# Kernel optimization log

Measured on AMD Instinct MI355X. Metric: run time of the kernel, lower is better.

## Reference

```python
import jax, jax.numpy as jnp
import numpy as np

N_SEARCH, B, C, H, W = 10, 32, 768, 24, 24
HT, WT = 8, 8
HEADS, POOL = 12, 4


def _G(t):
    # Integral of the bilinear triangle kernel: G(t) = int_{-1}^{t} max(0,1-|s|) ds
    tc = jnp.clip(t, -1.0, 1.0)
    return 0.5 + tc * (1.0 - 0.5 * jnp.abs(tc))


def prroi_pool(feats, rois, pool):
    # feats: [R,C,H,W], rois: [R,4] pixel coords (x0,y0,x1,y1); exact PrRoIPool2D
    R, C_, H_, W_ = feats.shape
    x0, y0, x1, y1 = rois[:, 0], rois[:, 1], rois[:, 2], rois[:, 3]
    bw = (x1 - x0) / pool
    bh = (y1 - y0) / pool
    p = jnp.arange(pool, dtype=feats.dtype)
    ex0 = x0[:, None] + p[None, :] * bw[:, None]   # [R,pool]
    ex1 = ex0 + bw[:, None]
    ey0 = y0[:, None] + p[None, :] * bh[:, None]
    ey1 = ey0 + bh[:, None]
    ix = jnp.arange(W_, dtype=feats.dtype)
    iy = jnp.arange(H_, dtype=feats.dtype)
    wx = _G(ex1[:, :, None] - ix) - _G(ex0[:, :, None] - ix)  # [R,pool,W]
    wy = _G(ey1[:, :, None] - iy) - _G(ey0[:, :, None] - iy)  # [R,pool,H]
    area = jnp.maximum(bw * bh, 1e-8)[:, None, None, None]
    return jnp.einsum('rph,rqw,rchw->rcpq', wy, wx, feats) / area  # [R,C,pool,pool]


def layernorm(x, g, b, eps=1e-5):
    m = jnp.mean(x, -1, keepdims=True)
    v = jnp.mean((x - m) ** 2, -1, keepdims=True)
    return (x - m) * jax.lax.rsqrt(v + eps) * g + b


def setup_inputs():
    key = jax.random.key(0)
    ks = jax.random.split(key, 24)
    search_feats = jax.random.normal(ks[0], (N_SEARCH, B, C, H, W), jnp.float32)
    template_feat = jax.random.normal(ks[1], (N_SEARCH, B, C, HT, WT), jnp.float32)
    u = jax.random.uniform(ks[2], (N_SEARCH, B, 4), jnp.float32)
    x0 = 0.05 + 0.4 * u[..., 0]
    y0 = 0.05 + 0.4 * u[..., 1]
    x1 = x0 + 0.15 + 0.3 * u[..., 2]
    y1 = y0 + 0.15 + 0.3 * u[..., 3]
    search_boxes = jnp.stack([x0, y0, x1, y1], -1)  # normalized, x1>x0, y1>y0
    s = 0.02
    d = {
        'search_feats': search_feats,
        'template_feat': template_feat,
        'search_boxes': search_boxes,
        'score_token': s * jax.random.normal(ks[3], (1, 1, C), jnp.float32),
        'ln1_g': jnp.ones((C,), jnp.float32), 'ln1_b': jnp.zeros((C,), jnp.float32),
        'Wq': s * jax.random.normal(ks[4], (2, C, C), jnp.float32), 'bq': jnp.zeros((2, C), jnp.float32),
        'Wk': s * jax.random.normal(ks[5], (2, C, C), jnp.float32), 'bk': jnp.zeros((2, C), jnp.float32),
        'Wv': s * jax.random.normal(ks[6], (2, C, C), jnp.float32), 'bv': jnp.zeros((2, C), jnp.float32),
        'Wo': s * jax.random.normal(ks[7], (2, C, C), jnp.float32), 'bo': jnp.zeros((2, C), jnp.float32),
        'ln2_g': jnp.ones((2, C), jnp.float32), 'ln2_b': jnp.zeros((2, C), jnp.float32),
        'Wmix': s * jax.random.normal(ks[8], (2, N_SEARCH, N_SEARCH), jnp.float32),
        'bmix': jnp.zeros((2, N_SEARCH), jnp.float32),
        'W1': s * jax.random.normal(ks[9], (C, C), jnp.float32), 'b1': jnp.zeros((C,), jnp.float32),
        'W2': s * jax.random.normal(ks[10], (C, C), jnp.float32), 'b2': jnp.zeros((C,), jnp.float32),
        'W3': s * jax.random.normal(ks[11], (C, 1), jnp.float32), 'b3': jnp.zeros((1,), jnp.float32),
    }
    return d


def reference(search_feats, template_feat, search_boxes, score_token, ln1_g, ln1_b,
              Wq, bq, Wk, bk, Wv, bv, Wo, bo, ln2_g, ln2_b, Wmix, bmix,
              W1, b1, W2, b2, W3, b3):
    N, b, c, h, w = search_feats.shape
    heads, pool = HEADS, POOL
    dh = c // heads
    scale = c ** (-0.5)  # note: full hidden_dim scale, as in original

    boxes = (search_boxes * w).reshape(-1, 4)              # [N*b,4] pixel coords
    feats = search_feats.reshape(-1, c, h, w)              # [N*b,c,h,w]
    pooled = prroi_pool(feats, boxes, pool)                # [N*b,c,pool,pool]
    # 'b c h w -> b (h w) c' then split N
    sbf = pooled.reshape(N, b, c, pool * pool).transpose(0, 1, 3, 2)  # [N,b,16,c]
    tmpl = template_feat.reshape(N, b, c, -1).transpose(0, 1, 3, 2)   # [N,b,64,c]

    x = jnp.broadcast_to(score_token, (N, b, 1, c))
    x = layernorm(x, ln1_g, ln1_b)
    kv = [sbf, tmpl]
    for i in range(2):
        q = x @ Wq[i] + bq[i]                              # [N,b,1,c]
        k = kv[i] @ Wk[i] + bk[i]                          # [N,b,T,c]
        v = kv[i] @ Wv[i] + bv[i]
        T = k.shape[2]
        qh = q.reshape(N, b, 1, heads, dh).transpose(0, 1, 3, 2, 4)   # [N,b,H,1,d]
        kh = k.reshape(N, b, T, heads, dh).transpose(0, 1, 3, 2, 4)   # [N,b,H,T,d]
        vh = v.reshape(N, b, T, heads, dh).transpose(0, 1, 3, 2, 4)
        attn = jax.nn.softmax(jnp.einsum('nbhld,nbhtd->nbhlt', qh, kh) * scale, -1)
        o = jnp.einsum('nbhlt,nbhtd->nbhld', attn, vh)
        o = o.transpose(0, 1, 3, 2, 4).reshape(N, b, 1, c)
        o = layernorm(o @ Wo[i] + bo[i], ln2_g[i], ln2_b[i])
        # time-mix across the N frames: [N,b,1,c] -> [b,c,N] -> linear -> [N,b,1,c]
        t = o[:, :, 0, :].transpose(1, 2, 0)               # [b,c,N]
        t = t @ Wmix[i] + bmix[i]
        x = t.transpose(2, 0, 1)[:, :, None, :]            # [N,b,1,c]

    hdd = jax.nn.relu(x @ W1 + b1)
    hdd = jax.nn.relu(hdd @ W2 + b2)
    return hdd @ W3 + b3                                   # [N,b,1,1]
```

## Files before the change

kernel.cpp:

```cpp
#include <hip/hip_runtime.h>
#include <cstdint>
#include <cstddef>

namespace {

constexpr float kScale = 0.03608439182435161f;
constexpr float kEps   = 1e-5f;

constexpr size_t OFF_QK0T = 0;
constexpr size_t OFF_QBK0 = 9216;
constexpr size_t OFF_S    = 16384;
constexpr size_t OFF_QK1  = OFF_S   + 2949120;
constexpr size_t OFF_O    = OFF_QK1 + 2949120;
constexpr size_t OFF_U    = OFF_O   + 245760;
constexpr size_t OFF_X    = OFF_U   + 245760;
constexpr size_t OFF_QF1  = OFF_X   + 245760;
constexpr size_t OFF_H1   = OFF_QF1 + 245760;
constexpr size_t OFF_H2   = OFF_H1  + 245760;

__device__ __forceinline__ float Gf(float t){
    float tc = fminf(fmaxf(t, -1.f), 1.f);
    return 0.5f + tc * (1.f - 0.5f * fabsf(tc));
}

__device__ __forceinline__ float blockReduce256(float v, float* red){
    #pragma unroll
    for (int off = 1; off < 64; off <<= 1) v += __shfl_xor(v, off);
    __syncthreads();
    if ((threadIdx.x & 63) == 0) red[threadIdx.x >> 6] = v;
    __syncthreads();
    return red[0] + red[1] + red[2] + red[3];
}

__global__ __launch_bounds__(256) void k_prep(
        const float* __restrict__ token, const float* __restrict__ g1,
        const float* __restrict__ b1,    const float* __restrict__ Wq0,
        const float* __restrict__ bq0,   const float* __restrict__ Wk0,
        const float* __restrict__ bk0,
        float* __restrict__ qk0T, float* __restrict__ qbk0){
    __shared__ float x0l[768];
    __shared__ float red[8];
    __shared__ float qfp[4][64];
    __shared__ float qfl[64];
    __shared__ float Ws[64][68];
    const int h  = blockIdx.x / 12;
    const int ct = blockIdx.x % 12;
    const int tid = threadIdx.x;

    float v0 = token[tid], v1 = token[tid+256], v2 = token[tid+512];
    float s = blockReduce256(v0+v1+v2, red);
    float m = s * (1.f/768.f);
    float d0 = v0-m, d1 = v1-m, d2 = v2-m;
    float qv = blockReduce256(d0*d0+d1*d1+d2*d2, red);
    float rs = rsqrtf(qv*(1.f/768.f) + kEps);
    x0l[tid]     = d0*rs*g1[tid]     + b1[tid];
    x0l[tid+256] = d1*rs*g1[tid+256] + b1[tid+256];
    x0l[tid+512] = d2*rs*g1[tid+512] + b1[tid+512];
    __syncthreads();

    {
        int dl = tid & 63, part = tid >> 6;
        int d = h*64 + dl;
        float a = 0.f;
        for (int c = part*192; c < part*192 + 192; ++c)
            a += x0l[c] * Wq0[(size_t)c*768 + d];
        qfp[part][dl] = a;
    }
    __syncthreads();
    if (tid < 64){
        int d = h*64 + tid;
        qfl[tid] = qfp[0][tid]+qfp[1][tid]+qfp[2][tid]+qfp[3][tid] + bq0[d];
    }
    __syncthreads();
    if (ct == 0 && tid < 64){
        float v = qfl[tid] * bk0[h*64 + tid];
        #pragma unroll
        for (int off = 1; off < 64; off <<= 1) v += __shfl_xor(v, off);
        if (tid == 0) qbk0[h] = v;
    }
    #pragma unroll
    for (int i = 0; i < 4; ++i){
        int f = tid + i*256; int cl = f >> 4, dd = (f & 15)*4;
        float4 v = *(const float4*)(Wk0 + (size_t)(ct*64+cl)*768 + h*64 + dd);
        *(float4*)&Ws[cl][dd] = v;
    }
    __syncthreads();
    {
        int cl = tid >> 2, part = tid & 3;
        float a = 0.f;
        #pragma unroll
        for (int jj = 0; jj < 16; ++jj){
            int dd = part*16 + jj;
            a += Ws[cl][dd] * qfl[dd];
        }
        a += __shfl_xor(a, 1); a += __shfl_xor(a, 2);
        if (part == 0) qk0T[h*768 + ct*64 + cl] = a;
    }
}

__global__ __launch_bounds__(256) void k_pool(
        const float* __restrict__ feats, const float* __restrict__ boxes,
        const float* __restrict__ qk0T,  const float* __restrict__ qbk0g,
        float* __restrict__ s0){
    __shared__ float P2[16][776];
    __shared__ float wxp[24][4];
    __shared__ float wyp[24][4];
    __shared__ float logitsL[12][17];
    __shared__ float attnT[16][12];
    __shared__ int   rng[4];
    __shared__ float areaInvS;
    const int r = blockIdx.x, tid = threadIdx.x;

    float bx0 = boxes[r*4+0]*24.f, by0 = boxes[r*4+1]*24.f;
    float bx1 = boxes[r*4+2]*24.f, by1 = boxes[r*4+3]*24.f;
    float bw = (bx1-bx0)*0.25f, bh = (by1-by0)*0.25f;
    if (tid == 0){
        int hlo = (int)floorf(by0) - 1; if (hlo < 0) hlo = 0;
        int hhi = (int)floorf(by1) + 1; if (hhi > 23) hhi = 23;
        int wlo = (int)floorf(bx0) - 1; if (wlo < 0) wlo = 0;
        int whi = (int)floorf(bx1) + 1; if (whi > 23) whi = 23;
        rng[0] = hlo; rng[1] = hhi; rng[2] = wlo >> 2; rng[3] = whi >> 2;
        areaInvS = 1.f / fmaxf(bw*bh, 1e-8f);
    }
    if (tid < 24){
        int w = tid;
        #pragma unroll
        for (int q = 0; q < 4; ++q){
            float e0 = bx0 + q*bw, e1 = e0 + bw;
            wxp[w][q] = Gf(e1 - (float)w) - Gf(e0 - (float)w);
        }
    } else if (tid < 48){
        int hh = tid - 24;
        #pragma unroll
        for (int p = 0; p < 4; ++p){
            float e0 = by0 + p*bh, e1 = e0 + bh;
            wyp[hh][p] = Gf(e1 - (float)hh) - Gf(e0 - (float)hh);
        }
    }
    __syncthreads();
    const int hlo = rng[0], hhi = rng[1], w4lo = rng[2], w4hi = rng[3];
    const float aInv = areaInvS;
    const int j = tid & 7;
    const int cbase = tid >> 3;

    for (int cg = 0; cg < 24; ++cg){
        int c = cg*32 + cbase;
        const float* fb = feats + ((size_t)r*768 + c)*576;
        float acc[16];
        #pragma unroll
        for (int k = 0; k < 16; ++k) acc[k] = 0.f;
        for (int hh = hlo + j; hh <= hhi; hh += 8){
            const float* rowp = fb + hh*24;
            float z[4] = {0.f,0.f,0.f,0.f};
            for (int w4 = w4lo; w4 <= w4hi; ++w4){
                float4 xv = *(const float4*)(rowp + w4*4);
                float xa[4] = {xv.x, xv.y, xv.z, xv.w};
                #pragma unroll
                for (int k = 0; k < 4; ++k){
                    float4 wv = *(const float4*)&wxp[w4*4+k][0];
                    z[0] += wv.x*xa[k]; z[1] += wv.y*xa[k];
                    z[2] += wv.z*xa[k]; z[3] += wv.w*xa[k];
                }
            }
            float4 wyv = *(const float4*)&wyp[hh][0];
            float wya[4] = {wyv.x, wyv.y, wyv.z, wyv.w};
            #pragma unroll
            for (int p = 0; p < 4; ++p)
                #pragma unroll
                for (int q = 0; q < 4; ++q)
                    acc[p*4+q] += wya[p]*z[q];
        }
        #pragma unroll
        for (int k = 0; k < 16; ++k){
            acc[k] += __shfl_xor(acc[k], 1);
            acc[k] += __shfl_xor(acc[k], 2);
            acc[k] += __shfl_xor(acc[k], 4);
        }
        P2[j][c]   = acc[j]   * aInv;
        P2[j+8][c] = acc[j+8] * aInv;
    }
    __syncthreads();

    if (tid < 192){
        int h = tid >> 4, t = tid & 15;
        float a = qbk0g[h];
        const float* qrow = qk0T + h*768;
        #pragma unroll 4
        for (int c4 = 0; c4 < 192; ++c4){
            float4 qv = *(const float4*)(qrow + c4*4);
            float4 pv = *(const float4*)&P2[t][c4*4];
            a += qv.x*pv.x + qv.y*pv.y + qv.z*pv.z + qv.w*pv.w;
        }
        logitsL[h][t] = a * kScale;
    }
    __syncthreads();
    if (tid < 12){
        float mx = -1e30f;
        for (int t = 0; t < 16; ++t) mx = fmaxf(mx, logitsL[tid][t]);
        float ss = 0.f;
        for (int t = 0; t < 16; ++t){
            float e = expf(logitsL[tid][t] - mx);
            attnT[t][tid] = e; ss += e;
        }
        float rsn = 1.f/ss;
        for (int t = 0; t < 16; ++t) attnT[t][tid] *= rsn;
    }
    __syncthreads();
    #pragma unroll
    for (int s3 = 0; s3 < 3; ++s3){
        int c = tid + s3*256;
        float a12[12];
        #pragma unroll
        for (int h = 0; h < 12; ++h) a12[h] = 0.f;
        #pragma unroll
        for (int t = 0; t < 16; ++t){
            float x = P2[t][c];
            float4 a0 = *(const float4*)&attnT[t][0];
            float4 a1 = *(const float4*)&attnT[t][4];
            float4 a2 = *(const float4*)&attnT[t][8];
            a12[0] += a0.x*x; a12[1] += a0.y*x; a12[2]  += a0.z*x; a12[3]  += a0.w*x;
            a12[4] += a1.x*x; a12[5] += a1.y*x; a12[6]  += a1.z*x; a12[7]  += a1.w*x;
            a12[8] += a2.x*x; a12[9] += a2.y*x; a12[10] += a2.z*x; a12[11] += a2.w*x;
        }
        #pragma unroll
        for (int h = 0; h < 12; ++h)
            s0[((size_t)r*12 + h)*768 + c] = a12[h];
    }
}

template<int HG, int RELU>
__global__ __launch_bounds__(256) void k_gemm(
        const float* __restrict__ A, const float* __restrict__ B,
        const float* __restrict__ bias, float* __restrict__ C){
    __shared__ float As[16][68];
    __shared__ float Bs[64][68];
    const int m0 = blockIdx.x * 16;
    const int n0 = blockIdx.y * 64;
    const int h  = blockIdx.y;
    const int tid = threadIdx.x;
    const int tn = tid & 15, tm = tid >> 4;
    float acc[4] = {0.f,0.f,0.f,0.f};

    for (int kt = 0; kt < 768; kt += 64){
        {
            int ml = tid >> 4, kk = (tid & 15)*4;
            const float* src = HG ? (A + ((size_t)(m0+ml)*12 + h)*768 + kt + kk)
                                  : (A + (size_t)(m0+ml)*768 + kt + kk);
            *(float4*)&As[ml][kk] = *(const float4*)src;
        }
        #pragma unroll
        for (int i = 0; i < 4; ++i){
            int f = tid + i*256;
            int kl = f >> 4, nn = (f & 15)*4;
            *(float4*)&Bs[kl][nn] =
                *(const float4*)(B + (size_t)(kt+kl)*768 + n0 + nn);
        }
        __syncthreads();
        #pragma unroll
        for (int k4 = 0; k4 < 16; ++k4){
            float4 av = *(const float4*)&As[tm][k4*4];
            float aa[4] = {av.x, av.y, av.z, av.w};
            #pragma unroll
            for (int jj = 0; jj < 4; ++jj){
                float4 bv = *(const float4*)&Bs[k4*4+jj][tn*4];
                acc[0] += aa[jj]*bv.x; acc[1] += aa[jj]*bv.y;
                acc[2] += aa[jj]*bv.z; acc[3] += aa[jj]*bv.w;
            }
        }
        __syncthreads();
    }
    int n = n0 + tn*4;
    float4 bb = *(const float4*)(bias + n);
    acc[0] += bb.x; acc[1] += bb.y; acc[2] += bb.z; acc[3] += bb.w;
    if (RELU){
        acc[0] = fmaxf(acc[0],0.f); acc[1] = fmaxf(acc[1],0.f);
        acc[2] = fmaxf(acc[2],0.f); acc[3] = fmaxf(acc[3],0.f);
    }
    float4 outv; outv.x = acc[0]; outv.y = acc[1]; outv.z = acc[2]; outv.w = acc[3];
    *(float4*)(C + (size_t)(m0+tm)*768 + n) = outv;
}

__global__ __launch_bounds__(256) void k_qk1(
        const float* __restrict__ qf1, const float* __restrict__ Wk1,
        float* __restrict__ qk1){
    __shared__ float As[32][68];
    __shared__ float Bs[64][68];
    const int r0 = blockIdx.x * 32, h = blockIdx.y, c0 = blockIdx.z * 64;
    const int tid = threadIdx.x;
    #pragma unroll
    for (int i = 0; i < 2; ++i){
        int f = tid + i*256; int ml = f >> 4, kk = (f & 15)*4;
        *(float4*)&As[ml][kk] =
            *(const float4*)(qf1 + (size_t)(r0+ml)*768 + h*64 + kk);
    }
    #pragma unroll
    for (int i = 0; i < 4; ++i){
        int f = tid + i*256; int cl = f >> 4, dd = (f & 15)*4;
        float4 v = *(const float4*)(Wk1 + (size_t)(c0+cl)*768 + h*64 + dd);
        Bs[dd+0][cl] = v.x; Bs[dd+1][cl] = v.y;
        Bs[dd+2][cl] = v.z; Bs[dd+3][cl] = v.w;
    }
    __syncthreads();
    const int tn = tid & 15, tm = tid >> 4;
    float acc0[4] = {0.f,0.f,0.f,0.f};
    float acc1[4] = {0.f,0.f,0.f,0.f};
    #pragma unroll
    for (int k4 = 0; k4 < 16; ++k4){
        float4 av0 = *(const float4*)&As[tm*2+0][k4*4];
        float4 av1 = *(const float4*)&As[tm*2+1][k4*4];
        float a0a[4] = {av0.x, av0.y, av0.z, av0.w};
        float a1a[4] = {av1.x, av1.y, av1.z, av1.w};
        #pragma unroll
        for (int jj = 0; jj < 4; ++jj){
            float4 bv = *(const float4*)&Bs[k4*4+jj][tn*4];
            acc0[0] += a0a[jj]*bv.x; acc0[1] += a0a[jj]*bv.y;
            acc0[2] += a0a[jj]*bv.z; acc0[3] += a0a[jj]*bv.w;
            acc1[0] += a1a[jj]*bv.x; acc1[1] += a1a[jj]*bv.y;
            acc1[2] += a1a[jj]*bv.z; acc1[3] += a1a[jj]*bv.w;
        }
    }
    float4 o0; o0.x=acc0[0]; o0.y=acc0[1]; o0.z=acc0[2]; o0.w=acc0[3];
    float4 o1; o1.x=acc1[0]; o1.y=acc1[1]; o1.z=acc1[2]; o1.w=acc1[3];
    *(float4*)(qk1 + ((size_t)(r0+tm*2+0)*12 + h)*768 + c0 + tn*4) = o0;
    *(float4*)(qk1 + ((size_t)(r0+tm*2+1)*12 + h)*768 + c0 + tn*4) = o1;
}

__global__ __launch_bounds__(256) void k_attn1(
        const float* __restrict__ tmpl, const float* __restrict__ qf1,
        const float* __restrict__ bk1,  const float* __restrict__ qk1,
        float* __restrict__ s1){
    __shared__ float Tc[192][68];
    __shared__ float logitsT[64][13];
    __shared__ float attnH[12][64];
    __shared__ float qbk[12];
    const int r = blockIdx.x, tid = threadIdx.x;
    const float* tp = tmpl + (size_t)r*768*64;

    if (tid < 192){
        int h = tid >> 4, pp = tid & 15;
        float v = 0.f;
        #pragma unroll
        for (int jj = 0; jj < 4; ++jj){
            int d = h*64 + pp*4 + jj;
            v += bk1[d] * qf1[(size_t)r*768 + d];
        }
        v += __shfl_xor(v,1); v += __shfl_xor(v,2);
        v += __shfl_xor(v,4); v += __shfl_xor(v,8);
        if (pp == 0) qbk[h] = v;
    }
    __syncthreads();
    float lacc[3];
    #pragma unroll
    for (int s = 0; s < 3; ++s){
        int task = tid + s*256;
        lacc[s] = qbk[task >> 6];
    }
    for (int cb = 0; cb < 4; ++cb){
        #pragma unroll
        for (int i = 0; i < 12; ++i){
            int f = tid + i*256; int cl = f >> 4, t4 = (f & 15)*4;
            *(float4*)&Tc[cl][t4] =
                *(const float4*)(tp + (size_t)(cb*192 + cl)*64 + t4);
        }
        __syncthreads();
        #pragma unroll
        for (int s = 0; s < 3; ++s){
            int task = tid + s*256;
            int h = task >> 6, t = task & 63;
            const float* qrow = qk1 + ((size_t)r*12 + h)*768 + cb*192;
            float a = 0.f;
            #pragma unroll 4
            for (int c4 = 0; c4 < 48; ++c4){
                float4 qv = *(const float4*)(qrow + c4*4);
                a += qv.x*Tc[c4*4+0][t] + qv.y*Tc[c4*4+1][t]
                   + qv.z*Tc[c4*4+2][t] + qv.w*Tc[c4*4+3][t];
            }
            lacc[s] += a;
        }
        __syncthreads();
    }
    #pragma unroll
    for (int s = 0; s < 3; ++s){
        int task = tid + s*256;
        logitsT[task & 63][task >> 6] = lacc[s] * kScale;
    }
    __syncthreads();
    if (tid < 12){
        float mx = -1e30f;
        for (int t = 0; t < 64; ++t) mx = fmaxf(mx, logitsT[t][tid]);
        float ss = 0.f;
        for (int t = 0; t < 64; ++t){
            float e = expf(logitsT[t][tid] - mx);
            attnH[tid][t] = e; ss += e;
        }
        float rsn = 1.f/ss;
        for (int t = 0; t < 64; ++t) attnH[tid][t] *= rsn;
    }
    __syncthreads();
    for (int cb = 0; cb < 4; ++cb){
        #pragma unroll
        for (int i = 0; i < 12; ++i){
            int f = tid + i*256; int cl = f >> 4, t4 = (f & 15)*4;
            *(float4*)&Tc[cl][t4] =
                *(const float4*)(tp + (size_t)(cb*192 + cl)*64 + t4);
        }
        __syncthreads();
        if (tid < 192){
            float4 trow[16];
            #pragma unroll
            for (int t4 = 0; t4 < 16; ++t4)
                trow[t4] = *(const float4*)&Tc[tid][t4*4];
            int c = cb*192 + tid;
            #pragma unroll
            for (int h = 0; h < 12; ++h){
                float a = 0.f;
                #pragma unroll
                for (int t4 = 0; t4 < 16; ++t4){
                    float4 avv = *(const float4*)&attnH[h][t4*4];
                    float4 tv = trow[t4];
                    a += avv.x*tv.x + avv.y*tv.y + avv.z*tv.z + avv.w*tv.w;
                }
                s1[((size_t)r*12 + h)*768 + c] = a;
            }
        }
        __syncthreads();
    }
}

__global__ __launch_bounds__(256) void k_lnmix(
        const float* __restrict__ u, const float* __restrict__ g,
        const float* __restrict__ bta, const float* __restrict__ Wmix,
        const float* __restrict__ bmix, float* __restrict__ xout){
    __shared__ float lnl[10][768];
    __shared__ float red[8];
    __shared__ float wm[100];
    __shared__ float bm[10];
    const int b = blockIdx.x, tid = threadIdx.x;
    if (tid < 100) wm[tid] = Wmix[tid];
    if (tid < 10)  bm[tid] = bmix[tid];
    for (int n = 0; n < 10; ++n){
        const float* row = u + (size_t)(n*32 + b)*768;
        float v0 = row[tid], v1 = row[tid+256], v2 = row[tid+512];
        float s = blockReduce256(v0+v1+v2, red);
        float m = s * (1.f/768.f);
        float d0 = v0-m, d1 = v1-m, d2 = v2-m;
        float qv = blockReduce256(d0*d0+d1*d1+d2*d2, red);
        float rs = rsqrtf(qv*(1.f/768.f) + kEps);
        lnl[n][tid]     = d0*rs*g[tid]     + bta[tid];
        lnl[n][tid+256] = d1*rs*g[tid+256] + bta[tid+256];
        lnl[n][tid+512] = d2*rs*g[tid+512] + bta[tid+512];
    }
    __syncthreads();
    #pragma unroll
    for (int s3 = 0; s3 < 3; ++s3){
        int c = tid + s3*256;
        float col[10];
        #pragma unroll
        for (int n = 0; n < 10; ++n) col[n] = lnl[n][c];
        #pragma unroll
        for (int np = 0; np < 10; ++np){
            float a = bm[np];
            #pragma unroll
            for (int n = 0; n < 10; ++n) a += col[n]*wm[n*10+np];
            xout[(size_t)(np*32 + b)*768 + c] = a;
        }
    }
}

__global__ __launch_bounds__(256) void k_head(
        const float* __restrict__ h2v, const float* __restrict__ W3,
        const float* __restrict__ b3, float* __restrict__ out){
    __shared__ float red[8];
    const int r = blockIdx.x, tid = threadIdx.x;
    const float* row = h2v + (size_t)r*768;
    float a = row[tid]*W3[tid] + row[tid+256]*W3[tid+256] + row[tid+512]*W3[tid+512];
    a = blockReduce256(a, red);
    if (tid == 0) out[r] = a + b3[0];
}

}

extern "C" void kernel_launch(void* const* d_in, const int* in_sizes, int n_in,
                              void* d_out, int out_size, void* d_ws, size_t ws_size,
                              hipStream_t stream){
    const float* feats = (const float*)d_in[0];
    const float* tmpl  = (const float*)d_in[1];
    const float* boxes = (const float*)d_in[2];
    const float* token = (const float*)d_in[3];
    const float* ln1g  = (const float*)d_in[4];
    const float* ln1b  = (const float*)d_in[5];
    const float* Wq    = (const float*)d_in[6];
    const float* bq    = (const float*)d_in[7];
    const float* Wk    = (const float*)d_in[8];
    const float* bk    = (const float*)d_in[9];
    const float* Wv    = (const float*)d_in[10];
    const float* bv    = (const float*)d_in[11];
    const float* Wo    = (const float*)d_in[12];
    const float* bo    = (const float*)d_in[13];
    const float* ln2g  = (const float*)d_in[14];
    const float* ln2b  = (const float*)d_in[15];
    const float* Wmix  = (const float*)d_in[16];
    const float* bmix  = (const float*)d_in[17];
    const float* W1    = (const float*)d_in[18];
    const float* b1v   = (const float*)d_in[19];
    const float* W2    = (const float*)d_in[20];
    const float* b2v   = (const float*)d_in[21];
    const float* W3    = (const float*)d_in[22];
    const float* b3v   = (const float*)d_in[23];
    float* ws  = (float*)d_ws;
    float* out = (float*)d_out;

    float* qk0T = ws + OFF_QK0T;
    float* qbk0 = ws + OFF_QBK0;
    float* sbuf = ws + OFF_S;
    float* qk1  = ws + OFF_QK1;
    float* obuf = ws + OFF_O;
    float* ubuf = ws + OFF_U;
    float* xbuf = ws + OFF_X;
    float* qf1  = ws + OFF_QF1;
    float* h1b  = ws + OFF_H1;
    float* h2b  = ws + OFF_H2;

    const size_t MO = 589824;

    k_prep<<<144, 256, 0, stream>>>(token, ln1g, ln1b, Wq, bq, Wk, bk, qk0T, qbk0);
    k_pool<<<320, 256, 0, stream>>>(feats, boxes, qk0T, qbk0, sbuf);
    k_gemm<1,0><<<dim3(20,12), 256, 0, stream>>>(sbuf, Wv, bv, obuf);
    k_gemm<0,0><<<dim3(20,12), 256, 0, stream>>>(obuf, Wo, bo, ubuf);
    k_lnmix<<<32, 256, 0, stream>>>(ubuf, ln2g, ln2b, Wmix, bmix, xbuf);
    k_gemm<0,0><<<dim3(20,12), 256, 0, stream>>>(xbuf, Wq + MO, bq + 768, qf1);
    k_qk1<<<dim3(10,12,12), 256, 0, stream>>>(qf1, Wk + MO, qk1);
    k_attn1<<<320, 256, 0, stream>>>(tmpl, qf1, bk + 768, qk1, sbuf);
    k_gemm<1,0><<<dim3(20,12), 256, 0, stream>>>(sbuf, Wv + MO, bv + 768, obuf);
    k_gemm<0,0><<<dim3(20,12), 256, 0, stream>>>(obuf, Wo + MO, bo + 768, ubuf);
    k_lnmix<<<32, 256, 0, stream>>>(ubuf, ln2g + 768, ln2b + 768, Wmix + 100, bmix + 10, xbuf);
    k_gemm<0,1><<<dim3(20,12), 256, 0, stream>>>(xbuf, W1, b1v, h1b);
    k_gemm<0,1><<<dim3(20,12), 256, 0, stream>>>(h1b, W2, b2v, h2b);
    k_head<<<320, 256, 0, stream>>>(h2b, W3, b3v, out);
}
```

Baseline: 414.0 us.

## Replace FP32 SIMT GEMMs with split-bf16 MFMA GEMMs using pre-packed weights

Adds a weight-prep kernel that splits each 768x768 weight matrix into high and low bf16 parts and packs them into MFMA fragment layout. The seven dense GEMMs now use a new kernel that also splits activations into hi/lo bf16 and runs three bf16 MFMAs per tile to approximate FP32 accuracy, with double-buffered LDS for A and register prefetch for B. This targets the FP32 FMA cost of the small-M GEMMs. In exchange it adds a weight-conversion launch every call, extra workspace, and slightly reduced precision from dropping the lo*lo term.

```diff
diff --git a/kernel.cpp b/kernel.cpp
--- a/kernel.cpp
+++ b/kernel.cpp
@@ -17,6 +17,22 @@
 constexpr size_t OFF_QF1  = OFF_X   + 245760;
 constexpr size_t OFF_H1   = OFF_QF1 + 245760;
 constexpr size_t OFF_H2   = OFF_H1  + 245760;
+constexpr size_t OFF_WF   = OFF_H2  + 245760;
+
+constexpr size_t WF_MAT_SHORTS = 1179648;
+
+typedef short short8v __attribute__((ext_vector_type(8)));
+typedef float float4v __attribute__((ext_vector_type(4)));
+
+union BP  { int4 i4; short8v s8; };
+union S4P { int2 i2; short s[4]; };
+
+__device__ __forceinline__ void splitBf(float a, short &h, short &l){
+    unsigned u = __float_as_uint(a);
+    h = (short)(u >> 16);
+    float r = a - __uint_as_float(u & 0xFFFF0000u);
+    l = (short)(__float_as_uint(r) >> 16);
+}
 
 __device__ __forceinline__ float Gf(float t){
     float tc = fminf(fmaxf(t, -1.f), 1.f);
@@ -30,6 +46,118 @@
     if ((threadIdx.x & 63) == 0) red[threadIdx.x >> 6] = v;
     __syncthreads();
     return red[0] + red[1] + red[2] + red[3];
+}
+
+__global__ __launch_bounds__(256) void k_wprep(
+        const float* __restrict__ w0, const float* __restrict__ w1,
+        const float* __restrict__ w2, const float* __restrict__ w3,
+        const float* __restrict__ w4, const float* __restrict__ w5,
+        const float* __restrict__ w6, short* __restrict__ WF){
+    const float* Wsel[7] = {w0,w1,w2,w3,w4,w5,w6};
+    const float* W = Wsel[blockIdx.y];
+    const int unit = blockIdx.x * 4 + (threadIdx.x >> 6);
+    const int l = threadIdx.x & 63;
+    const int kt = unit / 48, nb = unit % 48;
+    const int n = nb*16 + (l & 15);
+    const int kb = kt*32 + ((l >> 4) << 2);
+    S4P hi0, hi1, lo0, lo1;
+    #pragma unroll
+    for (int e = 0; e < 4; ++e){
+        float a = W[(size_t)(kb + e) * 768 + n];
+        splitBf(a, hi0.s[e], lo0.s[e]);
+        float b = W[(size_t)(kb + 16 + e) * 768 + n];
+        splitBf(b, hi1.s[e], lo1.s[e]);
+    }
+    size_t base = (size_t)blockIdx.y * WF_MAT_SHORTS + (size_t)unit * 1024 + (size_t)l * 8;
+    *(int2*)(WF + base)            = hi0.i2;
+    *(int2*)(WF + base + 4)        = hi1.i2;
+    *(int2*)(WF + base + 512)      = lo0.i2;
+    *(int2*)(WF + base + 512 + 4)  = lo1.i2;
+}
+
+template<int HG, int RELU>
+__global__ __launch_bounds__(256) void k_mgemm(
+        const float* __restrict__ A, const short* __restrict__ WFm,
+        const float* __restrict__ bias, float* __restrict__ C){
+    __shared__ short AF[2][2][2][64][8];
+    const int h   = blockIdx.y;
+    const int m0  = blockIdx.x * 32;
+    const int tid = threadIdx.x;
+    const int l   = tid & 63;
+    const int w   = tid >> 6;
+    const int wm  = w >> 1, wn = w & 1;
+
+    const int srow = tid >> 3, sk4 = tid & 7;
+    const int sfm  = srow >> 4;
+    const int slane = (srow & 15) + 16 * (sk4 & 3);
+    const int sebase = 4 * (sk4 >> 2);
+    const float* aRow = HG ? (A + ((size_t)(m0 + srow) * 12 + h) * 768)
+                           : (A + (size_t)(m0 + srow) * 768);
+
+    const int nb0 = h * 4 + wn * 2;
+    const short* WB = WFm + (size_t)nb0 * 1024 + (size_t)l * 8;
+
+    float4v acc0 = {0.f,0.f,0.f,0.f};
+    float4v acc1 = {0.f,0.f,0.f,0.f};
+
+    {
+        float4 a0 = *(const float4*)(aRow + sk4 * 4);
+        S4P hi, lo;
+        splitBf(a0.x, hi.s[0], lo.s[0]); splitBf(a0.y, hi.s[1], lo.s[1]);
+        splitBf(a0.z, hi.s[2], lo.s[2]); splitBf(a0.w, hi.s[3], lo.s[3]);
+        *(int2*)&AF[0][sfm][0][slane][sebase] = hi.i2;
+        *(int2*)&AF[0][sfm][1][slane][sebase] = lo.i2;
+    }
+    BP bh0, bl0, bh1, bl1;
+    bh0.i4 = *(const int4*)(WB);
+    bl0.i4 = *(const int4*)(WB + 512);
+    bh1.i4 = *(const int4*)(WB + 1024);
+    bl1.i4 = *(const int4*)(WB + 1536);
+    __syncthreads();
+
+    #pragma unroll 1
+    for (int kt = 0; kt < 24; ++kt){
+        const int cur = kt & 1;
+        const int ktn = (kt < 23) ? kt + 1 : 23;
+        float4 aN = *(const float4*)(aRow + ktn * 32 + sk4 * 4);
+        BP cbh0 = bh0, cbl0 = bl0, cbh1 = bh1, cbl1 = bl1;
+        {
+            const short* wb = WB + (size_t)ktn * 49152;
+            bh0.i4 = *(const int4*)(wb);
+            bl0.i4 = *(const int4*)(wb + 512);
+            bh1.i4 = *(const int4*)(wb + 1024);
+            bl1.i4 = *(const int4*)(wb + 1536);
+        }
+        short8v ah = *(short8v*)&AF[cur][wm][0][l][0];
+        short8v al = *(short8v*)&AF[cur][wm][1][l][0];
+        acc0 = __builtin_amdgcn_mfma_f32_16x16x32_bf16(ah, cbh0.s8, acc0, 0, 0, 0);
+        acc0 = __builtin_amdgcn_mfma_f32_16x16x32_bf16(al, cbh0.s8, acc0, 0, 0, 0);
+        acc0 = __builtin_amdgcn_mfma_f32_16x16x32_bf16(ah, cbl0.s8, acc0, 0, 0, 0);
+        acc1 = __builtin_amdgcn_mfma_f32_16x16x32_bf16(ah, cbh1.s8, acc1, 0, 0, 0);
+        acc1 = __builtin_amdgcn_mfma_f32_16x16x32_bf16(al, cbh1.s8, acc1, 0, 0, 0);
+        acc1 = __builtin_amdgcn_mfma_f32_16x16x32_bf16(ah, cbl1.s8, acc1, 0, 0, 0);
+        if (kt < 23){
+            S4P hi, lo;
+            splitBf(aN.x, hi.s[0], lo.s[0]); splitBf(aN.y, hi.s[1], lo.s[1]);
+            splitBf(aN.z, hi.s[2], lo.s[2]); splitBf(aN.w, hi.s[3], lo.s[3]);
+            *(int2*)&AF[cur ^ 1][sfm][0][slane][sebase] = hi.i2;
+            *(int2*)&AF[cur ^ 1][sfm][1][slane][sebase] = lo.i2;
+        }
+        __syncthreads();
+    }
+
+    const int col0 = h * 64 + (wn * 2 + 0) * 16 + (l & 15);
+    const int col1 = h * 64 + (wn * 2 + 1) * 16 + (l & 15);
+    const float b0 = bias[col0], b1 = bias[col1];
+    #pragma unroll
+    for (int reg = 0; reg < 4; ++reg){
+        int row = m0 + wm * 16 + ((l >> 4) << 2) + reg;
+        float v0 = acc0[reg] + b0;
+        float v1 = acc1[reg] + b1;
+        if (RELU){ v0 = fmaxf(v0, 0.f); v1 = fmaxf(v1, 0.f); }
+        C[(size_t)row * 768 + col0] = v0;
+        C[(size_t)row * 768 + col1] = v1;
+    }
 }
 
 __global__ __launch_bounds__(256) void k_prep(
@@ -226,58 +354,6 @@
         for (int h = 0; h < 12; ++h)
             s0[((size_t)r*12 + h)*768 + c] = a12[h];
     }
-}
-
-template<int HG, int RELU>
-__global__ __launch_bounds__(256) void k_gemm(
-        const float* __restrict__ A, const float* __restrict__ B,
-        const float* __restrict__ bias, float* __restrict__ C){
-    __shared__ float As[16][68];
-    __shared__ float Bs[64][68];
-    const int m0 = blockIdx.x * 16;
-    const int n0 = blockIdx.y * 64;
-    const int h  = blockIdx.y;
-    const int tid = threadIdx.x;
-    const int tn = tid & 15, tm = tid >> 4;
-    float acc[4] = {0.f,0.f,0.f,0.f};
-
-    for (int kt = 0; kt < 768; kt += 64){
-        {
-            int ml = tid >> 4, kk = (tid & 15)*4;
-            const float* src = HG ? (A + ((size_t)(m0+ml)*12 + h)*768 + kt + kk)
-                                  : (A + (size_t)(m0+ml)*768 + kt + kk);
-            *(float4*)&As[ml][kk] = *(const float4*)src;
-        }
-        #pragma unroll
-        for (int i = 0; i < 4; ++i){
-            int f = tid + i*256;
-            int kl = f >> 4, nn = (f & 15)*4;
-            *(float4*)&Bs[kl][nn] =
-                *(const float4*)(B + (size_t)(kt+kl)*768 + n0 + nn);
-        }
-        __syncthreads();
-        #pragma unroll
-        for (int k4 = 0; k4 < 16; ++k4){
-            float4 av = *(const float4*)&As[tm][k4*4];
-            float aa[4] = {av.x, av.y, av.z, av.w};
-            #pragma unroll
-            for (int jj = 0; jj < 4; ++jj){
-                float4 bv = *(const float4*)&Bs[k4*4+jj][tn*4];
-                acc[0] += aa[jj]*bv.x; acc[1] += aa[jj]*bv.y;
-                acc[2] += aa[jj]*bv.z; acc[3] += aa[jj]*bv.w;
-            }
-        }
-        __syncthreads();
-    }
-    int n = n0 + tn*4;
-    float4 bb = *(const float4*)(bias + n);
-    acc[0] += bb.x; acc[1] += bb.y; acc[2] += bb.z; acc[3] += bb.w;
-    if (RELU){
-        acc[0] = fmaxf(acc[0],0.f); acc[1] = fmaxf(acc[1],0.f);
-        acc[2] = fmaxf(acc[2],0.f); acc[3] = fmaxf(acc[3],0.f);
-    }
-    float4 outv; outv.x = acc[0]; outv.y = acc[1]; outv.z = acc[2]; outv.w = acc[3];
-    *(float4*)(C + (size_t)(m0+tm)*768 + n) = outv;
 }
 
 __global__ __launch_bounds__(256) void k_qk1(
@@ -520,21 +596,30 @@
     float* qf1  = ws + OFF_QF1;
     float* h1b  = ws + OFF_H1;
     float* h2b  = ws + OFF_H2;
+    short* wf   = (short*)(ws + OFF_WF);
 
     const size_t MO = 589824;
-
+    short* wfv0 = wf + 0*WF_MAT_SHORTS;
+    short* wfo0 = wf + 1*WF_MAT_SHORTS;
+    short* wfq1 = wf + 2*WF_MAT_SHORTS;
+    short* wfv1 = wf + 3*WF_MAT_SHORTS;
+    short* wfo1 = wf + 4*WF_MAT_SHORTS;
+    short* wf1  = wf + 5*WF_MAT_SHORTS;
+    short* wf2  = wf + 6*WF_MAT_SHORTS;
+
+    k_wprep<<<dim3(288,7), 256, 0, stream>>>(Wv, Wo, Wq + MO, Wv + MO, Wo + MO, W1, W2, wf);
     k_prep<<<144, 256, 0, stream>>>(token, ln1g, ln1b, Wq, bq, Wk, bk, qk0T, qbk0);
     k_pool<<<320, 256, 0, stream>>>(feats, boxes, qk0T, qbk0, sbuf);
-    k_gemm<1,0><<<dim3(20,12), 256, 0, stream>>>(sbuf, Wv, bv, obuf);
-    k_gemm<0,0><<<dim3(20,12), 256, 0, stream>>>(obuf, Wo, bo, ubuf);
+    k_mgemm<1,0><<<dim3(10,12), 256, 0, stream>>>(sbuf, wfv0, bv, obuf);
+    k_mgemm<0,0><<<dim3(10,12), 256, 0, stream>>>(obuf, wfo0, bo, ubuf);
     k_lnmix<<<32, 256, 0, stream>>>(ubuf, ln2g, ln2b, Wmix, bmix, xbuf);
-    k_gemm<0,0><<<dim3(20,12), 256, 0, stream>>>(xbuf, Wq + MO, bq + 768, qf1);
+    k_mgemm<0,0><<<dim3(10,12), 256, 0, stream>>>(xbuf, wfq1, bq + 768, qf1);
     k_qk1<<<dim3(10,12,12), 256, 0, stream>>>(qf1, Wk + MO, qk1);
     k_attn1<<<320, 256, 0, stream>>>(tmpl, qf1, bk + 768, qk1, sbuf);
-    k_gemm<1,0><<<dim3(20,12), 256, 0, stream>>>(sbuf, Wv + MO, bv + 768, obuf);
-    k_gemm<0,0><<<dim3(20,12), 256, 0, stream>>>(obuf, Wo + MO, bo + 768, ubuf);
+    k_mgemm<1,0><<<dim3(10,12), 256, 0, stream>>>(sbuf, wfv1, bv + 768, obuf);
+    k_mgemm<0,0><<<dim3(10,12), 256, 0, stream>>>(obuf, wfo1, bo + 768, ubuf);
     k_lnmix<<<32, 256, 0, stream>>>(ubuf, ln2g + 768, ln2b + 768, Wmix + 100, bmix + 10, xbuf);
-    k_gemm<0,1><<<dim3(20,12), 256, 0, stream>>>(xbuf, W1, b1v, h1b);
-    k_gemm<0,1><<<dim3(20,12), 256, 0, stream>>>(h1b, W2, b2v, h2b);
+    k_mgemm<0,1><<<dim3(10,12), 256, 0, stream>>>(xbuf, wf1, b1v, h1b);
+    k_mgemm<0,1><<<dim3(10,12), 256, 0, stream>>>(h1b, wf2, b2v, h2b);
     k_head<<<320, 256, 0, stream>>>(h2b, W3, b3v, out);
 }
```

Measured after the change: 424.6 us. 1.03x slower.
